# Kernel optimization log

Hardware: AMD Instinct MI355X
Metric: run time of the kernel (lower is better)

Reference implementation:

```python
import jax, jax.numpy as jnp
import numpy as np

L, D, H, KVH, DH, F, V, SMAX, T = 4, 2048, 16, 8, 128, 6144, 32000, 2048, 1024
EPS = 1e-6
ROPE_THETA = 1e6


def rotate_half(x, axis=-1):
    x1, x2 = jnp.split(x, 2, axis=axis)
    return jnp.concatenate((-x2, x1), axis=axis)


def rms(x, w):
    return w * (x / jnp.sqrt(jnp.mean(x * x, axis=-1, keepdims=True) + EPS))


def setup_inputs() -> dict:
    key = jax.random.key(0)
    ks = jax.random.split(key, 16)
    s = 0.02
    inv_freq = 1.0 / (ROPE_THETA ** (jnp.arange(0, DH, 2, dtype=jnp.float32) / DH))
    ang = jnp.arange(SMAX, dtype=jnp.float32)[:, None] * inv_freq[None, :]  # [SMAX, DH/2]
    cos_emb = jnp.concatenate([jnp.cos(ang), jnp.cos(ang)], axis=-1)  # [SMAX, DH]
    sin_emb = jnp.concatenate([jnp.sin(ang), jnp.sin(ang)], axis=-1)
    sf = DH ** (-0.25)  # scale_factor pre-baked into q_norm/k_norm weights
    return {
        "key_buffer": jnp.zeros((L, KVH, 1, DH, SMAX), jnp.float32),
        "value_buffer": jnp.zeros((L, KVH, 1, SMAX, DH), jnp.float32),
        "input_ids": jax.random.randint(ks[0], (1, T), 0, V, dtype=jnp.int32),
        "attention_mask": jnp.ones((1, T, T), jnp.float32),
        "past_len": 0,
        "embed_data": jax.random.randint(ks[1], (V, D), 0, 256).astype(jnp.uint8),
        "embed_scale": jax.random.uniform(ks[2], (V, 1), jnp.float32, 0.001, 0.02),
        "embed_zero": jax.random.normal(ks[3], (V, 1), jnp.float32) * 0.1,
        "cos_emb": cos_emb,
        "sin_emb": sin_emb,
        "w_in_ln": jnp.ones((L, D), jnp.float32),
        "Wq": jax.random.normal(ks[4], (L, D, H * DH), jnp.float32) * s,
        "Wk": jax.random.normal(ks[5], (L, D, KVH * DH), jnp.float32) * s,
        "Wv": jax.random.normal(ks[6], (L, D, KVH * DH), jnp.float32) * s,
        "w_q_norm": jnp.full((L, DH), sf, jnp.float32),
        "w_k_norm": jnp.full((L, DH), sf, jnp.float32),
        "Wo": jax.random.normal(ks[7], (L, H * DH, D), jnp.float32) * s,
        "w_post_ln": jnp.ones((L, D), jnp.float32),
        "Wgate": jax.random.normal(ks[8], (L, D, F), jnp.float32) * s,
        "Wup": jax.random.normal(ks[9], (L, D, F), jnp.float32) * s,
        "Wdown": jax.random.normal(ks[10], (L, F, D), jnp.float32) * s,
        "w_final_norm": jnp.ones((D,), jnp.float32),
        "W_lm": jax.random.normal(ks[11], (D, V), jnp.float32) * s,
    }


def reference(key_buffer, value_buffer, input_ids, attention_mask, past_len,
              embed_data, embed_scale, embed_zero, cos_emb, sin_emb,
              w_in_ln, Wq, Wk, Wv, w_q_norm, w_k_norm, Wo, w_post_ln,
              Wgate, Wup, Wdown, w_final_norm, W_lm):
    new_len = input_ids.shape[1]
    end = past_len + new_len  # static (past_len is a Python int)
    cos_q = cos_emb[past_len:end]  # [T, DH]
    sin_q = sin_emb[past_len:end]
    # uint8 embedding dequant: e * scale + zero_point
    hidden = embed_data[input_ids].astype(jnp.float32) * embed_scale[input_ids] + embed_zero[input_ids]  # [1,T,D]
    # causal mask: (1 - tril) * -128, sliced to [1, new_len, end], times user mask
    rows = jnp.arange(new_len) + past_len
    cols = jnp.arange(end)
    mask = jnp.where(cols[None, :] <= rows[:, None], 0.0, -128.0)[None] * attention_mask  # [1,T,end]
    G = H // KVH
    for i in range(L):
        hn = rms(hidden, w_in_ln[i])[0]  # [T, D]
        q = (hn @ Wq[i]).reshape(new_len, H, DH)
        q = jnp.transpose(rms(q, w_q_norm[i]), (1, 0, 2))  # [H,T,DH] (sqrt(scale) baked in w_q_norm)
        k = (hn @ Wk[i]).reshape(new_len, KVH, DH)
        k = jnp.transpose(rms(k, w_k_norm[i]), (1, 2, 0))  # [KVH,DH,T]
        v = jnp.transpose((hn @ Wv[i]).reshape(new_len, KVH, DH), (1, 0, 2))  # [KVH,T,DH]
        # RoPE on keys (rotate along DH axis=1)
        k = k * cos_q.T + rotate_half(k, axis=1) * sin_q.T
        key_buffer = jax.lax.dynamic_update_slice(key_buffer, k[None, :, None], (i, 0, 0, 0, past_len))
        value_buffer = jax.lax.dynamic_update_slice(value_buffer, v[None, :, None], (i, 0, 0, past_len, 0))
        # GQA expand: each kv head repeated G times consecutively
        k_exp = jnp.repeat(key_buffer[i, :, 0, :, :end], G, axis=0)  # [H,DH,end]
        v_exp = jnp.repeat(value_buffer[i, :, 0, :end, :], G, axis=0)  # [H,end,DH]
        q_rot = q * cos_q[None] + rotate_half(q, axis=-1) * sin_q[None]
        scores = jnp.einsum('htd,hds->hts', q_rot, k_exp) + mask
        attn = jax.nn.softmax(scores, axis=-1)
        ctx = jnp.transpose(jnp.einsum('hts,hsd->htd', attn, v_exp), (1, 0, 2)).reshape(1, new_len, H * DH)
        hidden = hidden + ctx @ Wo[i]
        hn2 = rms(hidden, w_post_ln[i])
        hidden = hidden + (jax.nn.silu(hn2 @ Wgate[i]) * (hn2 @ Wup[i])) @ Wdown[i]
    last = rms(hidden[:, -1], w_final_norm)  # [1, D]
    logits = last @ W_lm  # [1, V]
    tok_id = jnp.argmax(logits, axis=-1, keepdims=True).astype(jnp.int32)
    new_seq_len = jnp.array([end], dtype=jnp.int32)
    return (tok_id, key_buffer, value_buffer, new_seq_len)
```

## Files before the change

kernel.cpp:

```cpp
#include <hip/hip_runtime.h>
#include <cstdint>

#define L_ 4
#define D_ 2048
#define H_ 16
#define KVH_ 8
#define DH_ 128
#define F_ 6144
#define V_ 32000
#define SMAX_ 2048
#define T_ 1024
#define EPS_ 1e-6f
#define QB 32
#define SB 128
#define ZSE 4194304

typedef unsigned short u16;
typedef unsigned int u32;
typedef float fvec4 __attribute__((ext_vector_type(4)));
typedef float f32x4 __attribute__((ext_vector_type(4)));
typedef __bf16 bf16x8 __attribute__((ext_vector_type(8)));

__device__ __forceinline__ u16 f2bf(float f) {
  union { float f; u32 u; } a; a.f = f;
  u32 u = a.u;
  return (u16)((u + 0x7FFFu + ((u >> 16) & 1u)) >> 16);
}

__device__ __forceinline__ void gld16(const void* g, void* l) {
  __builtin_amdgcn_global_load_lds(
      (const __attribute__((address_space(1))) void*)g,
      (__attribute__((address_space(3))) void*)l, 16, 0, 0);
}

__device__ __forceinline__ float blk_sum(float v, volatile float* sm) {
#pragma unroll
  for (int m = 32; m; m >>= 1) v += __shfl_xor(v, m);
  if ((threadIdx.x & 63) == 0) sm[threadIdx.x >> 6] = v;
  __syncthreads();
  v = sm[0] + sm[1] + sm[2] + sm[3];
  __syncthreads();
  return v;
}

__global__ void embed_k(const int* __restrict__ ids, const void* __restrict__ edata,
                        const float* __restrict__ esc, const float* __restrict__ ez,
                        float* __restrict__ hidden)
{
  const int* ei = (const int*)edata;
  int chk = ei[threadIdx.x & 63];
  bool ok = ((unsigned)chk) <= 255u;
  bool is_i32 = (__ballot(ok) == ~0ULL);
  int t = blockIdx.x;
  int id = ids[t];
  float sc = esc[id], zp = ez[id];
  size_t base = (size_t)id * D_;
  const uint8_t* eb = (const uint8_t*)edata;
  for (int d = threadIdx.x; d < D_; d += 256) {
    float e = is_i32 ? (float)ei[base + d] : (float)eb[base + d];
    hidden[(size_t)t * D_ + d] = e * sc + zp;
  }
}

__global__ __launch_bounds__(256)
void convT2_k(const float* __restrict__ W0, const float* __restrict__ W1,
              const float* __restrict__ W2,
              int x1, int x2, int N0, int N1, int N2,
              int r0, int r1, int r2, int K, u16* __restrict__ WT, int gu)
{
  __shared__ float tile[64][65];
  int x = blockIdx.x, k0 = blockIdx.y * 64;
  const float* W; int N, nb, rb;
  if (x < x1)      { W = W0; N = N0; nb = x;      rb = r0; }
  else if (x < x2) { W = W1; N = N1; nb = x - x1; rb = r1; }
  else             { W = W2; N = N2; nb = x - x2; rb = r2; }
  int n0 = nb * 64;
  int tid = threadIdx.x;
  int lk = tid >> 4, n4 = (tid & 15) * 4;
#pragma unroll
  for (int i = 0; i < 4; ++i) {
    int kr = i * 16 + lk;
    fvec4 v = *(const fvec4*)(W + (size_t)(k0 + kr) * N + n0 + n4);
#pragma unroll
    for (int j = 0; j < 4; ++j) tile[n4 + j][kr] = v[j];
  }
  __syncthreads();
  int n = tid >> 2, kq = (tid & 3) * 16;
  int f = n0 + n;
  int row = gu ? (rb + ((f >> 4) << 5) + (f & 15)) : (rb + f);
  union { u16 h[16]; uint4 q[2]; } o;
#pragma unroll
  for (int i = 0; i < 16; ++i) o.h[i] = f2bf(tile[n][kq + i]);
  u16* op = WT + (size_t)row * K + k0 + kq;
  *(uint4*)op = o.q[0];
  *(uint4*)(op + 8) = o.q[1];
}

template<int NZ>
__global__ __launch_bounds__(256)
void rms_k(float* __restrict__ x, const float* __restrict__ p,
           const float* __restrict__ w, u16* __restrict__ out)
{
  int t = blockIdx.x * 4 + (threadIdx.x >> 6);
  int l = threadIdx.x & 63;
  fvec4* xr = (fvec4*)(x + (size_t)t * D_);
  fvec4 v[8];
#pragma unroll
  for (int j = 0; j < 8; ++j) v[j] = xr[l + 64 * j];
  if (NZ > 0) {
#pragma unroll
    for (int z = 0; z < NZ; ++z) {
      const fvec4* a = (const fvec4*)(p + (size_t)z * ZSE + (size_t)t * D_);
#pragma unroll
      for (int j = 0; j < 8; ++j) v[j] += a[l + 64 * j];
    }
#pragma unroll
    for (int j = 0; j < 8; ++j) xr[l + 64 * j] = v[j];
  }
  float s = 0.f;
#pragma unroll
  for (int j = 0; j < 8; ++j)
    s += v[j][0]*v[j][0] + v[j][1]*v[j][1] + v[j][2]*v[j][2] + v[j][3]*v[j][3];
#pragma unroll
  for (int m = 32; m; m >>= 1) s += __shfl_xor(s, m);
  float inv = rsqrtf(s * (1.f / D_) + EPS_);
  const fvec4* wr = (const fvec4*)w;
  u16* orow = out + (size_t)t * D_;
#pragma unroll
  for (int j = 0; j < 8; ++j) {
    fvec4 wv = wr[l + 64 * j];
    uint2 o;
    o.x = (u32)f2bf(wv[0]*v[j][0]*inv) | ((u32)f2bf(wv[1]*v[j][1]*inv) << 16);
    o.y = (u32)f2bf(wv[2]*v[j][2]*inv) | ((u32)f2bf(wv[3]*v[j][3]*inv) << 16);
    *(uint2*)(orow + (l + 64 * j) * 4) = o;
  }
}

template<int EPI>
__global__ __launch_bounds__(256)
void gemm_bt(const u16* __restrict__ A, const u16* __restrict__ B,
             float* __restrict__ Cf, u16* __restrict__ Cb,
             int K, int Ks, int ldC, long long zStride)
{
  __shared__ u16 lA[128 * 64];
  __shared__ u16 lB[128 * 64];
  const u16* Ab = A + (size_t)blockIdx.y * 128 * K;
  const u16* Bb = B + (size_t)blockIdx.x * 128 * K;
  int kz = blockIdx.z * Ks;

  int tid = threadIdx.x;
  int l = tid & 63;
  int wid = tid >> 6;
  int wr = wid >> 1, wc = wid & 1;
  int lrow = l & 15, lk = l >> 4;

  f32x4 acc[4][4] = {};

  for (int k0 = 0; k0 < Ks; k0 += 64) {
#pragma unroll
    for (int r = 0; r < 4; ++r) {
      int c = r * 256 + tid;
      int row = c >> 3, g = c & 7;
      int kel = kz + k0 + ((g ^ (row & 7)) << 3);
      gld16(Ab + (size_t)row * K + kel, (char*)lA + c * 16);
      gld16(Bb + (size_t)row * K + kel, (char*)lB + c * 16);
    }
    __syncthreads();
#pragma unroll
    for (int kk = 0; kk < 2; ++kk) {
      bf16x8 av[4], bv[4];
      int kbyte = (kk * 32 + lk * 8) * 2;
#pragma unroll
      for (int m = 0; m < 4; ++m) {
        int row = wr * 64 + m * 16 + lrow;
        int byt = (row * 128 + kbyte) ^ ((row & 7) << 4);
        av[m] = *(const bf16x8*)((const char*)lA + byt);
      }
#pragma unroll
      for (int n = 0; n < 4; ++n) {
        int row = wc * 64 + n * 16 + lrow;
        int byt = (row * 128 + kbyte) ^ ((row & 7) << 4);
        bv[n] = *(const bf16x8*)((const char*)lB + byt);
      }
#pragma unroll
      for (int m = 0; m < 4; ++m)
#pragma unroll
        for (int n = 0; n < 4; ++n)
          acc[m][n] = __builtin_amdgcn_mfma_f32_16x16x32_bf16(av[m], bv[n], acc[m][n], 0, 0, 0);
    }
    __syncthreads();
  }

  int grow0 = blockIdx.y * 128 + wr * 64 + lk * 4;
  if (EPI == 3) {
    int fcol0 = blockIdx.x * 64 + wc * 32 + lrow;
#pragma unroll
    for (int m = 0; m < 4; ++m)
#pragma unroll
      for (int np = 0; np < 2; ++np)
#pragma unroll
        for (int r = 0; r < 4; ++r) {
          float g = acc[m][2 * np][r], u = acc[m][2 * np + 1][r];
          float val = g / (1.f + __expf(-g)) * u;
          Cb[(size_t)(grow0 + m * 16 + r) * ldC + fcol0 + np * 16] = f2bf(val);
        }
    return;
  }
  float* Cz = Cf + (long long)blockIdx.z * zStride;
  int gcol0 = blockIdx.x * 128 + wc * 64 + lrow;
#pragma unroll
  for (int m = 0; m < 4; ++m)
#pragma unroll
    for (int n = 0; n < 4; ++n)
#pragma unroll
      for (int r = 0; r < 4; ++r) {
        size_t off = (size_t)(grow0 + m * 16 + r) * ldC + gcol0 + n * 16;
        Cz[off] = acc[m][n][r];
      }
}

__global__ __launch_bounds__(256)
void qkvpost_k(const float* __restrict__ p0, const float* __restrict__ p1,
               const float* __restrict__ wq, const float* __restrict__ wk,
               const float* __restrict__ cosT, const float* __restrict__ sinT,
               const int* __restrict__ plp,
               u16* __restrict__ qr, u16* __restrict__ kr, u16* __restrict__ vT,
               float* __restrict__ key_out, float* __restrict__ val_out)
{
  __shared__ float tile[64][132];
  int t0 = blockIdx.x * 64;
  int z = blockIdx.y;
  int pl = plp[0];
  int tid = threadIdx.x;
  int cb = z < 16 ? z * 128 : (z < 24 ? 2048 + (z - 16) * 128 : 3072 + (z - 24) * 128);

  {
    int r = tid >> 5;
    int c = (tid & 31) * 4;
#pragma unroll
    for (int i = 0; i < 8; ++i) {
      int row = i * 8 + r;
      size_t off = (size_t)(t0 + row) * 4096 + cb + c;
      fvec4 v = *(const fvec4*)(p0 + off) + *(const fvec4*)(p1 + off);
      *(fvec4*)&tile[row][c] = v;
    }
  }
  __syncthreads();

  if (z < 24) {
    int row = tid >> 2, q = tid & 3;
    int dbase = q * 32, pbase = (q ^ 2) * 32;
    const float* wn = z < 16 ? wq : wk;
    float sgn = (q < 2) ? -1.f : 1.f;
    fvec4 xv[8];
    float ss = 0.f;
#pragma unroll
    for (int j = 0; j < 8; ++j) {
      xv[j] = *(const fvec4*)&tile[row][dbase + j * 4];
      ss += xv[j][0]*xv[j][0] + xv[j][1]*xv[j][1] + xv[j][2]*xv[j][2] + xv[j][3]*xv[j][3];
    }
    ss += __shfl_xor(ss, 1);
    ss += __shfl_xor(ss, 2);
    float inv = rsqrtf(ss * (1.f / 128.f) + EPS_);
    int p = pl + t0 + row;
    float rv[32];
#pragma unroll
    for (int j = 0; j < 8; ++j) {
      fvec4 xo = *(const fvec4*)&tile[row][pbase + j * 4];
      fvec4 wv = *(const fvec4*)(wn + dbase + j * 4);
      fvec4 wo = *(const fvec4*)(wn + pbase + j * 4);
      fvec4 cs = *(const fvec4*)(cosT + (size_t)p * 128 + dbase + j * 4);
      fvec4 sn = *(const fvec4*)(sinT + (size_t)p * 128 + dbase + j * 4);
#pragma unroll
      for (int e = 0; e < 4; ++e) {
        float xn = wv[e] * xv[j][e] * inv;
        float xp = wo[e] * xo[e] * inv;
        rv[j * 4 + e] = xn * cs[e] + sgn * xp * sn[e];
      }
    }
    union { u32 w[8]; uint4 q4[2]; } ob;
    u16* orow = (z < 16 ? qr + ((size_t)z * T_ + t0 + row) * 128
                        : kr + ((size_t)(z - 16) * T_ + t0 + row) * 128) + dbase;
#pragma unroll
    for (int j = 0; j < 8; ++j)
      ob.w[j] = (u32)f2bf(rv[2 * j]) | ((u32)f2bf(rv[2 * j + 1]) << 16);
    *(uint4*)orow = ob.q4[0];
    *(uint4*)(orow + 8) = ob.q4[1];
#pragma unroll
    for (int j = 0; j < 8; ++j)
      ob.w[j] = (u32)f2bf(rv[16 + 2 * j]) | ((u32)f2bf(rv[17 + 2 * j]) << 16);
    *(uint4*)(orow + 16) = ob.q4[0];
    *(uint4*)(orow + 24) = ob.q4[1];

    if (z >= 16) {
      __syncthreads();
#pragma unroll
      for (int j = 0; j < 8; ++j) {
        fvec4 v; v[0] = rv[j*4]; v[1] = rv[j*4+1]; v[2] = rv[j*4+2]; v[3] = rv[j*4+3];
        *(fvec4*)&tile[row][dbase + j * 4] = v;
      }
      __syncthreads();
      int d = tid >> 1, cc = (tid & 1) * 32;
      float* kp = key_out + ((size_t)(z - 16) * 128 + d) * SMAX_ + pl + t0 + cc;
      if ((pl & 3) == 0) {
#pragma unroll
        for (int j4 = 0; j4 < 8; ++j4) {
          fvec4 v;
#pragma unroll
          for (int e = 0; e < 4; ++e) v[e] = tile[cc + j4 * 4 + e][d];
          *(fvec4*)(kp + j4 * 4) = v;
        }
      } else {
        for (int j = 0; j < 32; ++j) kp[j] = tile[cc + j][d];
      }
    }
  } else {
    int kv = z - 24;
    int row = tid >> 2, q = tid & 3;
    float* vp = val_out + ((size_t)kv * SMAX_ + pl + t0 + row) * 128 + q * 32;
#pragma unroll
    for (int j = 0; j < 8; ++j)
      *(fvec4*)(vp + j * 4) = *(const fvec4*)&tile[row][q * 32 + j * 4];
    int d = tid >> 1, cc = (tid & 1) * 32;
    union { u32 w[16]; uint4 q4[4]; } ob;
    u16* tp = vT + ((size_t)kv * 128 + d) * T_ + t0 + cc;
#pragma unroll
    for (int j = 0; j < 16; ++j)
      ob.w[j] = (u32)f2bf(tile[cc + 2 * j][d]) | ((u32)f2bf(tile[cc + 2 * j + 1][d]) << 16);
    *(uint4*)tp = ob.q4[0];
    *(uint4*)(tp + 8) = ob.q4[1];
    *(uint4*)(tp + 16) = ob.q4[2];
    *(uint4*)(tp + 24) = ob.q4[3];
  }
}

__global__ __launch_bounds__(256)
void flash_k(const u16* __restrict__ qr, const u16* __restrict__ kr,
             const u16* __restrict__ vTb, const float* __restrict__ am,
             const int* __restrict__ plp, u16* __restrict__ ctx)
{
  __shared__ u16 lQ[QB * DH_];
  __shared__ u16 lKV[SB * DH_];
  __shared__ u16 lP[QB * SB];
  __shared__ float lMax[2][2][16];
  __shared__ float lSum[2][2][16];
  __shared__ float lScale[QB];
  __shared__ float lFin[QB];

  int qt = gridDim.x - 1 - blockIdx.x;
  int h = blockIdx.y;
  int kvh = h >> 1;
  int pl = plp[0];
  int tid = threadIdx.x;
  int l = tid & 63, w = tid >> 6;
  int lrow = l & 15, lk = l >> 4;
  int tb = w & 1, sh = w >> 1;
  int tcol = tb * 16 + lrow;

  const u16* Qb = qr + ((size_t)h * T_ + qt * QB) * DH_;
  const u16* Kb = kr + (size_t)kvh * T_ * DH_;
  const u16* Vb = vTb + (size_t)kvh * DH_ * T_;

#pragma unroll
  for (int r = 0; r < 2; ++r) {
    int c = r * 256 + tid;
    int row = c >> 4, g = c & 15;
    gld16(Qb + (size_t)row * DH_ + ((g ^ (row & 7)) << 3), (char*)lQ + c * 16);
  }

  float m_run = -3.0e38f, l_run = 0.f;
  f32x4 acc_o[2][2] = {};

  int t_lo = qt * QB;
  int s_hi = min(T_, t_lo + QB + pl);
  int nt = (s_hi + SB - 1) / SB;
  int tg = t_lo + tcol;

  for (int it = 0; it < nt; ++it) {
    int s0 = it * SB;
#pragma unroll
    for (int r = 0; r < 8; ++r) {
      int c = r * 256 + tid;
      int row = c >> 4, g = c & 15;
      gld16(Kb + (size_t)(s0 + row) * DH_ + ((g ^ (row & 7)) << 3), (char*)lKV + c * 16);
    }
    __syncthreads();

    f32x4 acc_s[4] = {};
#pragma unroll
    for (int kk = 0; kk < 4; ++kk) {
      int kbyte = kk * 64 + lk * 16;
      int trow = tb * 16 + lrow;
      bf16x8 bq = *(const bf16x8*)((const char*)lQ + ((trow * 256 + kbyte) ^ ((trow & 7) << 4)));
#pragma unroll
      for (int m = 0; m < 4; ++m) {
        int srow = sh * 64 + m * 16 + lrow;
        bf16x8 ak = *(const bf16x8*)((const char*)lKV + ((srow * 256 + kbyte) ^ ((srow & 7) << 4)));
        acc_s[m] = __builtin_amdgcn_mfma_f32_16x16x32_bf16(ak, bq, acc_s[m], 0, 0, 0);
      }
    }
    __syncthreads();

#pragma unroll
    for (int r = 0; r < 8; ++r) {
      int c = r * 256 + tid;
      int row = c >> 4, g = c & 15;
      gld16(Vb + (size_t)row * T_ + s0 + ((g ^ (row & 7)) << 3), (char*)lKV + c * 16);
    }

    bool full = (s0 + SB <= t_lo + pl + 1);
    float sv[4][4];
    float vmax = -3.0e38f;
    if (full) {
#pragma unroll
      for (int m = 0; m < 4; ++m)
#pragma unroll
        for (int r = 0; r < 4; ++r) {
          float val = acc_s[m][r]; sv[m][r] = val; vmax = fmaxf(vmax, val);
        }
    } else {
#pragma unroll
      for (int m = 0; m < 4; ++m) {
        int sg = s0 + sh * 64 + m * 16 + lk * 4;
        fvec4 a4 = *(const fvec4*)(am + (size_t)tg * T_ + sg);
#pragma unroll
        for (int r = 0; r < 4; ++r) {
          float val = acc_s[m][r] + ((sg + r <= tg + pl) ? 0.f : -128.f * a4[r]);
          sv[m][r] = val; vmax = fmaxf(vmax, val);
        }
      }
    }
    vmax = fmaxf(vmax, __shfl_xor(vmax, 16));
    vmax = fmaxf(vmax, __shfl_xor(vmax, 32));
    if (lk == 0) lMax[tb][sh][lrow] = vmax;
    __syncthreads();

    float om = fmaxf(lMax[tb][0][lrow], lMax[tb][1][lrow]);
    float m_new = fmaxf(m_run, om);
    float corr = __expf(m_run - m_new);
    float psum = 0.f;
    u32 pw[4][2];
#pragma unroll
    for (int m = 0; m < 4; ++m) {
      float p0 = __expf(sv[m][0] - m_new);
      float p1 = __expf(sv[m][1] - m_new);
      float p2 = __expf(sv[m][2] - m_new);
      float p3 = __expf(sv[m][3] - m_new);
      psum += (p0 + p1) + (p2 + p3);
      pw[m][0] = (u32)f2bf(p0) | ((u32)f2bf(p1) << 16);
      pw[m][1] = (u32)f2bf(p2) | ((u32)f2bf(p3) << 16);
    }
    psum += __shfl_xor(psum, 16);
    psum += __shfl_xor(psum, 32);
    if (lk == 0) lSum[tb][sh][lrow] = psum;
    if (lk == 0 && sh == 0) lScale[tcol] = corr;
#pragma unroll
    for (int m = 0; m < 4; ++m) {
      int byt = (tcol * 256 + sh * 128 + m * 32 + lk * 8) ^ ((tcol & 7) << 4);
      *(uint2*)((char*)lP + byt) = make_uint2(pw[m][0], pw[m][1]);
    }
    __syncthreads();

    l_run = l_run * corr + lSum[tb][0][lrow] + lSum[tb][1][lrow];
    m_run = m_new;
#pragma unroll
    for (int m = 0; m < 2; ++m) {
      fvec4 c4 = *(const fvec4*)&lScale[m * 16 + lk * 4];
#pragma unroll
      for (int n = 0; n < 2; ++n)
#pragma unroll
        for (int r = 0; r < 4; ++r) acc_o[m][n][r] *= c4[r];
    }
#pragma unroll
    for (int kk = 0; kk < 4; ++kk) {
      int kbyte = kk * 64 + lk * 16;
      bf16x8 ap[2], bv[2];
#pragma unroll
      for (int m = 0; m < 2; ++m) {
        int trow = m * 16 + lrow;
        ap[m] = *(const bf16x8*)((const char*)lP + ((trow * 256 + kbyte) ^ ((trow & 7) << 4)));
      }
#pragma unroll
      for (int n = 0; n < 2; ++n) {
        int drow = w * 32 + n * 16 + lrow;
        bv[n] = *(const bf16x8*)((const char*)lKV + ((drow * 256 + kbyte) ^ ((drow & 7) << 4)));
      }
#pragma unroll
      for (int m = 0; m < 2; ++m)
#pragma unroll
        for (int n = 0; n < 2; ++n)
          acc_o[m][n] = __builtin_amdgcn_mfma_f32_16x16x32_bf16(ap[m], bv[n], acc_o[m][n], 0, 0, 0);
    }
    __syncthreads();
  }

  if (lk == 0 && sh == 0) lFin[tcol] = l_run;
  __syncthreads();
#pragma unroll
  for (int m = 0; m < 2; ++m) {
    fvec4 s4 = *(const fvec4*)&lFin[m * 16 + lk * 4];
#pragma unroll
    for (int r = 0; r < 4; ++r) {
      float inv = 1.f / s4[r];
      int trow = t_lo + m * 16 + lk * 4 + r;
      u16* crow = ctx + (size_t)trow * (H_ * DH_) + h * DH_;
#pragma unroll
      for (int n = 0; n < 2; ++n) {
        int d = w * 32 + n * 16 + lrow;
        crow[d] = f2bf(acc_o[m][n][r] * inv);
      }
    }
  }
}

__global__ void frms_k(const float* __restrict__ x, const float* __restrict__ p,
                       const float* __restrict__ w, float* __restrict__ out)
{
  __shared__ float sm[4];
  float s = 0.f;
  for (int d = threadIdx.x; d < D_; d += 256) {
    float v = x[d] + p[d] + p[ZSE + d] + p[2 * ZSE + d] + p[3 * ZSE + d];
    s += v * v;
  }
  s = blk_sum(s, sm);
  float inv = rsqrtf(s * (1.f / D_) + EPS_);
  for (int d = threadIdx.x; d < D_; d += 256)
    out[d] = w[d] * (x[d] + p[d] + p[ZSE + d] + p[2 * ZSE + d] + p[3 * ZSE + d]) * inv;
}

__global__ void lmgemv_k(const float* __restrict__ last, const float* __restrict__ Wlm,
                         float* __restrict__ part)
{
  __shared__ float ls[256];
  int v = blockIdx.x * 256 + threadIdx.x;
  int c = blockIdx.y;
  ls[threadIdx.x] = last[c * 256 + threadIdx.x];
  __syncthreads();
  const float* Wp = Wlm + (size_t)c * 256 * V_ + v;
  float acc = 0.f;
#pragma unroll 8
  for (int d = 0; d < 256; d++) acc += ls[d] * Wp[(size_t)d * V_];
  part[(size_t)c * V_ + v] = acc;
}

__global__ void amax_part_k(const float* __restrict__ part, float2* __restrict__ out)
{
  __shared__ float sv[4];
  __shared__ int si[4];
  int v = blockIdx.x * 256 + threadIdx.x;
  float val = 0.f;
#pragma unroll
  for (int c = 0; c < 8; c++) val += part[(size_t)c * V_ + v];
  float bv = val; int bi = v;
#pragma unroll
  for (int m = 32; m; m >>= 1) {
    float ov = __shfl_xor(bv, m);
    int oi = __shfl_xor(bi, m);
    if (ov > bv || (ov == bv && oi < bi)) { bv = ov; bi = oi; }
  }
  if ((threadIdx.x & 63) == 0) { sv[threadIdx.x >> 6] = bv; si[threadIdx.x >> 6] = bi; }
  __syncthreads();
  if (threadIdx.x == 0) {
    for (int w = 1; w < 4; w++)
      if (sv[w] > bv || (sv[w] == bv && si[w] < bi)) { bv = sv[w]; bi = si[w]; }
    out[blockIdx.x] = make_float2(bv, (float)bi);
  }
}

__global__ void finalize_k(const float2* __restrict__ part, int np,
                           const int* __restrict__ plp, float* __restrict__ dout,
                           unsigned long long lastoff)
{
  if (threadIdx.x == 0) {
    float bv = part[0].x; int bi = (int)part[0].y;
    for (int b = 1; b < np; b++) {
      float v = part[b].x; int i = (int)part[b].y;
      if (v > bv || (v == bv && i < bi)) { bv = v; bi = i; }
    }
    dout[0] = (float)bi;
    dout[lastoff] = (float)(plp[0] + T_);
  }
}

extern "C" void kernel_launch(void* const* d_in, const int* in_sizes, int n_in,
                              void* d_out, int out_size, void* d_ws, size_t ws_size,
                              hipStream_t stream)
{
  (void)in_sizes; (void)n_in; (void)out_size; (void)ws_size;

  const float* key_in  = (const float*)d_in[0];
  const float* val_in  = (const float*)d_in[1];
  const int*   ids     = (const int*)d_in[2];
  const float* am      = (const float*)d_in[3];
  const int*   plp     = (const int*)d_in[4];
  const void*  edata   = d_in[5];
  const float* esc     = (const float*)d_in[6];
  const float* ez      = (const float*)d_in[7];
  const float* cosT    = (const float*)d_in[8];
  const float* sinT    = (const float*)d_in[9];
  const float* w_in_ln = (const float*)d_in[10];
  const float* Wq      = (const float*)d_in[11];
  const float* Wk      = (const float*)d_in[12];
  const float* Wv      = (const float*)d_in[13];
  const float* wqn     = (const float*)d_in[14];
  const float* wkn     = (const float*)d_in[15];
  const float* Wo      = (const float*)d_in[16];
  const float* wpost   = (const float*)d_in[17];
  const float* Wg      = (const float*)d_in[18];
  const float* Wu      = (const float*)d_in[19];
  const float* Wd      = (const float*)d_in[20];
  const float* wfin    = (const float*)d_in[21];
  const float* Wlm     = (const float*)d_in[22];

  float* out = (float*)d_out;
  const size_t KVN = (size_t)L_ * KVH_ * DH_ * SMAX_;
  float* key_out = out + 1;
  float* val_out = out + 1 + KVN;
  unsigned long long lastoff = 1 + 2 * KVN;

  char* ws = (char*)d_ws;
  u16*   wT     = (u16*)  (ws + 0);
  u16*   hn     = (u16*)  (ws + 50331648);
  float* P      = (float*)(ws + 54525952);
  u16*   qr     = (u16*)  (ws + 121634816);
  u16*   kr     = (u16*)  (ws + 125829120);
  u16*   vT     = (u16*)  (ws + 127926272);
  u16*   ctx    = (u16*)  (ws + 130023424);
  float* hidden = (float*)(ws + 134217728);
  u16*   mlp    = (u16*)  (ws + 142606336);
  float* last   = (float*)(ws + 155189248);
  float* lpart  = (float*)(ws + 155197440);
  float2* amaxp = (float2*)(ws + 156221440);

  hipMemcpyAsync(key_out, key_in, KVN * sizeof(float), hipMemcpyDeviceToDevice, stream);
  hipMemcpyAsync(val_out, val_in, KVN * sizeof(float), hipMemcpyDeviceToDevice, stream);
  embed_k<<<T_, 256, 0, stream>>>(ids, edata, esc, ez, hidden);

  for (int i = 0; i < L_; i++) {
    if (i == 0)
      rms_k<0><<<T_ / 4, 256, 0, stream>>>(hidden, nullptr, w_in_ln, hn);
    else
      rms_k<4><<<T_ / 4, 256, 0, stream>>>(hidden, P, w_in_ln + (size_t)i * D_, hn);

    convT2_k<<<dim3(64, 32), 256, 0, stream>>>(
        Wq + (size_t)i * 4194304, Wk + (size_t)i * 2097152, Wv + (size_t)i * 2097152,
        32, 48, 2048, 1024, 1024, 0, 2048, 3072, 2048, wT, 0);
    gemm_bt<0><<<dim3(32, 8, 2), 256, 0, stream>>>(hn, wT, P, nullptr, 2048, 1024, 4096, ZSE);

    qkvpost_k<<<dim3(T_ / 64, 32), 256, 0, stream>>>(P, P + ZSE,
        wqn + (size_t)i * DH_, wkn + (size_t)i * DH_, cosT, sinT, plp,
        qr, kr, vT,
        key_out + (size_t)i * KVH_ * DH_ * SMAX_,
        val_out + (size_t)i * KVH_ * SMAX_ * DH_);

    flash_k<<<dim3(T_ / QB, H_), 256, 0, stream>>>(qr, kr, vT, am, plp, ctx);

    convT2_k<<<dim3(32, 32), 256, 0, stream>>>(
        Wo + (size_t)i * 4194304, nullptr, nullptr,
        32, 64, 2048, 2048, 2048, 0, 0, 0, 2048, wT, 0);
    gemm_bt<0><<<dim3(16, 8, 4), 256, 0, stream>>>(ctx, wT, P, nullptr, 2048, 512, 2048, ZSE);

    rms_k<4><<<T_ / 4, 256, 0, stream>>>(hidden, P, wpost + (size_t)i * D_, hn);

    convT2_k<<<dim3(192, 32), 256, 0, stream>>>(
        Wg + (size_t)i * 12582912, Wu + (size_t)i * 12582912, Wu + (size_t)i * 12582912,
        96, 192, 6144, 6144, 6144, 0, 16, 16, 2048, wT, 1);
    gemm_bt<3><<<dim3(96, 8, 1), 256, 0, stream>>>(hn, wT, nullptr, mlp, 2048, 2048, 6144, 0);

    convT2_k<<<dim3(32, 96), 256, 0, stream>>>(
        Wd + (size_t)i * 12582912, nullptr, nullptr,
        32, 64, 2048, 2048, 2048, 0, 0, 0, 6144, wT, 0);
    gemm_bt<0><<<dim3(16, 8, 4), 256, 0, stream>>>(mlp, wT, P, nullptr, 6144, 1536, 2048, ZSE);
  }

  frms_k<<<1, 256, 0, stream>>>(hidden + (size_t)(T_ - 1) * D_,
                                P + (size_t)(T_ - 1) * D_, wfin, last);
  lmgemv_k<<<dim3(V_ / 256, 8), 256, 0, stream>>>(last, Wlm, lpart);
  amax_part_k<<<V_ / 256, 256, 0, stream>>>(lpart, amaxp);
  finalize_k<<<1, 64, 0, stream>>>(amaxp, V_ / 256, plp, out, lastoff);
}
```

Before: 1.201 ms.

## Fuse weight transposes with RMS/qkv-post kernels and store split-K partials in bf16

```diff
diff --git a/kernel.cpp b/kernel.cpp
--- a/kernel.cpp
+++ b/kernel.cpp
@@ -26,21 +26,20 @@
   u32 u = a.u;
   return (u16)((u + 0x7FFFu + ((u >> 16) & 1u)) >> 16);
 }
+__device__ __forceinline__ float bf2f(u16 h) {
+  union { u32 u; float f; } a; a.u = (u32)h << 16; return a.f;
+}
+__device__ __forceinline__ fvec4 bf4(uint2 u) {
+  union { u32 i; float f; } a, b, c, d;
+  a.i = u.x << 16; b.i = u.x & 0xFFFF0000u;
+  c.i = u.y << 16; d.i = u.y & 0xFFFF0000u;
+  fvec4 r; r[0] = a.f; r[1] = b.f; r[2] = c.f; r[3] = d.f; return r;
+}
 
 __device__ __forceinline__ void gld16(const void* g, void* l) {
   __builtin_amdgcn_global_load_lds(
       (const __attribute__((address_space(1))) void*)g,
       (__attribute__((address_space(3))) void*)l, 16, 0, 0);
-}
-
-__device__ __forceinline__ float blk_sum(float v, volatile float* sm) {
-#pragma unroll
-  for (int m = 32; m; m >>= 1) v += __shfl_xor(v, m);
-  if ((threadIdx.x & 63) == 0) sm[threadIdx.x >> 6] = v;
-  __syncthreads();
-  v = sm[0] + sm[1] + sm[2] + sm[3];
-  __syncthreads();
-  return v;
 }
 
 __global__ void embed_k(const int* __restrict__ ids, const void* __restrict__ edata,
@@ -62,19 +61,11 @@
   }
 }
 
-__global__ __launch_bounds__(256)
-void convT2_k(const float* __restrict__ W0, const float* __restrict__ W1,
-              const float* __restrict__ W2,
-              int x1, int x2, int N0, int N1, int N2,
-              int r0, int r1, int r2, int K, u16* __restrict__ WT, int gu)
-{
-  __shared__ float tile[64][65];
-  int x = blockIdx.x, k0 = blockIdx.y * 64;
-  const float* W; int N, nb, rb;
-  if (x < x1)      { W = W0; N = N0; nb = x;      rb = r0; }
-  else if (x < x2) { W = W1; N = N1; nb = x - x1; rb = r1; }
-  else             { W = W2; N = N2; nb = x - x2; rb = r2; }
-  int n0 = nb * 64;
+__device__ __forceinline__ void convT_body(const float* __restrict__ W, int N,
+                                           int nb, int kb, int K, int rb,
+                                           u16* __restrict__ WT, int gu, float* tile)
+{
+  int n0 = nb * 64, k0 = kb * 64;
   int tid = threadIdx.x;
   int lk = tid >> 4, n4 = (tid & 15) * 4;
 #pragma unroll
@@ -82,7 +73,7 @@
     int kr = i * 16 + lk;
     fvec4 v = *(const fvec4*)(W + (size_t)(k0 + kr) * N + n0 + n4);
 #pragma unroll
-    for (int j = 0; j < 4; ++j) tile[n4 + j][kr] = v[j];
+    for (int j = 0; j < 4; ++j) tile[(n4 + j) * 65 + kr] = v[j];
   }
   __syncthreads();
   int n = tid >> 2, kq = (tid & 3) * 16;
@@ -90,18 +81,19 @@
   int row = gu ? (rb + ((f >> 4) << 5) + (f & 15)) : (rb + f);
   union { u16 h[16]; uint4 q[2]; } o;
 #pragma unroll
-  for (int i = 0; i < 16; ++i) o.h[i] = f2bf(tile[n][kq + i]);
+  for (int i = 0; i < 16; ++i) o.h[i] = f2bf(tile[n * 65 + kq + i]);
   u16* op = WT + (size_t)row * K + k0 + kq;
   *(uint4*)op = o.q[0];
   *(uint4*)(op + 8) = o.q[1];
 }
 
 template<int NZ>
-__global__ __launch_bounds__(256)
-void rms_k(float* __restrict__ x, const float* __restrict__ p,
-           const float* __restrict__ w, u16* __restrict__ out)
-{
-  int t = blockIdx.x * 4 + (threadIdx.x >> 6);
+__device__ __forceinline__ void rms_body(int idx, float* __restrict__ x,
+                                         const u16* __restrict__ p,
+                                         const float* __restrict__ w,
+                                         u16* __restrict__ out)
+{
+  int t = idx * 4 + (threadIdx.x >> 6);
   int l = threadIdx.x & 63;
   fvec4* xr = (fvec4*)(x + (size_t)t * D_);
   fvec4 v[8];
@@ -110,9 +102,9 @@
   if (NZ > 0) {
 #pragma unroll
     for (int z = 0; z < NZ; ++z) {
-      const fvec4* a = (const fvec4*)(p + (size_t)z * ZSE + (size_t)t * D_);
-#pragma unroll
-      for (int j = 0; j < 8; ++j) v[j] += a[l + 64 * j];
+      const uint2* a = (const uint2*)(p + (size_t)z * ZSE + (size_t)t * D_);
+#pragma unroll
+      for (int j = 0; j < 8; ++j) v[j] += bf4(a[l + 64 * j]);
     }
 #pragma unroll
     for (int j = 0; j < 8; ++j) xr[l + 64 * j] = v[j];
@@ -136,11 +128,52 @@
   }
 }
 
+template<int NZ>
+__global__ __launch_bounds__(256)
+void convqkv_rms_k(const float* __restrict__ Wq, const float* __restrict__ Wk,
+                   const float* __restrict__ Wv, u16* __restrict__ WT,
+                   float* __restrict__ x, const u16* __restrict__ p,
+                   const float* __restrict__ w, u16* __restrict__ out)
+{
+  __shared__ float tile[64 * 65];
+  int bx = blockIdx.x, y = blockIdx.y;
+  if (bx < 64) {
+    const float* W; int N, nb, rb;
+    if (bx < 32)      { W = Wq; N = 2048; nb = bx;      rb = 0; }
+    else if (bx < 48) { W = Wk; N = 1024; nb = bx - 32; rb = 2048; }
+    else              { W = Wv; N = 1024; nb = bx - 48; rb = 3072; }
+    convT_body(W, N, nb, y, 2048, rb, WT, 0, tile);
+  } else {
+    rms_body<NZ>((bx - 64) * 32 + y, x, p, w, out);
+  }
+}
+
+__global__ __launch_bounds__(256)
+void convgu_wd_rms_k(const float* __restrict__ Wg, const float* __restrict__ Wu,
+                     u16* __restrict__ WTgu, const float* __restrict__ Wd,
+                     u16* __restrict__ WTwd,
+                     float* __restrict__ x, const u16* __restrict__ p,
+                     const float* __restrict__ w, u16* __restrict__ out)
+{
+  __shared__ float tile[64 * 65];
+  int bx = blockIdx.x, y = blockIdx.y;
+  if (bx < 192) {
+    const float* W; int nb, rb;
+    if (bx < 96) { W = Wg; nb = bx;      rb = 0; }
+    else         { W = Wu; nb = bx - 96; rb = 16; }
+    convT_body(W, 6144, nb, y, 2048, rb, WTgu, 1, tile);
+  } else if (bx < 288) {
+    int xp = bx - 192;
+    convT_body(Wd, 2048, xp & 31, ((xp >> 5) << 5) + y, 6144, 0, WTwd, 0, tile);
+  } else {
+    rms_body<4>((bx - 288) * 32 + y, x, p, w, out);
+  }
+}
+
 template<int EPI>
 __global__ __launch_bounds__(256)
 void gemm_bt(const u16* __restrict__ A, const u16* __restrict__ B,
-             float* __restrict__ Cf, u16* __restrict__ Cb,
-             int K, int Ks, int ldC, long long zStride)
+             u16* __restrict__ Cb, int K, int Ks, int ldC, long long zStride)
 {
   __shared__ u16 lA[128 * 64];
   __shared__ u16 lB[128 * 64];
@@ -206,28 +239,31 @@
         }
     return;
   }
-  float* Cz = Cf + (long long)blockIdx.z * zStride;
+  u16* Cz = Cb + (long long)blockIdx.z * zStride;
   int gcol0 = blockIdx.x * 128 + wc * 64 + lrow;
 #pragma unroll
   for (int m = 0; m < 4; ++m)
 #pragma unroll
     for (int n = 0; n < 4; ++n)
 #pragma unroll
-      for (int r = 0; r < 4; ++r) {
-        size_t off = (size_t)(grow0 + m * 16 + r) * ldC + gcol0 + n * 16;
-        Cz[off] = acc[m][n][r];
-      }
+      for (int r = 0; r < 4; ++r)
+        Cz[(size_t)(grow0 + m * 16 + r) * ldC + gcol0 + n * 16] = f2bf(acc[m][n][r]);
 }
 
 __global__ __launch_bounds__(256)
-void qkvpost_k(const float* __restrict__ p0, const float* __restrict__ p1,
-               const float* __restrict__ wq, const float* __restrict__ wk,
-               const float* __restrict__ cosT, const float* __restrict__ sinT,
-               const int* __restrict__ plp,
-               u16* __restrict__ qr, u16* __restrict__ kr, u16* __restrict__ vT,
-               float* __restrict__ key_out, float* __restrict__ val_out)
+void qkvpost_convwo_k(const u16* __restrict__ p0, const u16* __restrict__ p1,
+                      const float* __restrict__ wq, const float* __restrict__ wk,
+                      const float* __restrict__ cosT, const float* __restrict__ sinT,
+                      const int* __restrict__ plp,
+                      u16* __restrict__ qr, u16* __restrict__ kr, u16* __restrict__ vT,
+                      float* __restrict__ key_out, float* __restrict__ val_out,
+                      const float* __restrict__ Wo, u16* __restrict__ WTo)
 {
   __shared__ float tile[64][132];
+  if (blockIdx.x >= 16) {
+    convT_body(Wo, 2048, blockIdx.x - 16, blockIdx.y, 2048, 0, WTo, 0, &tile[0][0]);
+    return;
+  }
   int t0 = blockIdx.x * 64;
   int z = blockIdx.y;
   int pl = plp[0];
@@ -241,7 +277,7 @@
     for (int i = 0; i < 8; ++i) {
       int row = i * 8 + r;
       size_t off = (size_t)(t0 + row) * 4096 + cb + c;
-      fvec4 v = *(const fvec4*)(p0 + off) + *(const fvec4*)(p1 + off);
+      fvec4 v = bf4(*(const uint2*)(p0 + off)) + bf4(*(const uint2*)(p1 + off));
       *(fvec4*)&tile[row][c] = v;
     }
   }
@@ -513,19 +549,23 @@
   }
 }
 
-__global__ void frms_k(const float* __restrict__ x, const float* __restrict__ p,
+__global__ void frms_k(const float* __restrict__ x, const u16* __restrict__ p,
                        const float* __restrict__ w, float* __restrict__ out)
 {
   __shared__ float sm[4];
   float s = 0.f;
   for (int d = threadIdx.x; d < D_; d += 256) {
-    float v = x[d] + p[d] + p[ZSE + d] + p[2 * ZSE + d] + p[3 * ZSE + d];
+    float v = x[d] + bf2f(p[d]) + bf2f(p[ZSE + d]) + bf2f(p[2 * ZSE + d]) + bf2f(p[3 * ZSE + d]);
     s += v * v;
   }
-  s = blk_sum(s, sm);
+#pragma unroll
+  for (int m = 32; m; m >>= 1) s += __shfl_xor(s, m);
+  if ((threadIdx.x & 63) == 0) sm[threadIdx.x >> 6] = s;
+  __syncthreads();
+  s = sm[0] + sm[1] + sm[2] + sm[3];
   float inv = rsqrtf(s * (1.f / D_) + EPS_);
   for (int d = threadIdx.x; d < D_; d += 256)
-    out[d] = w[d] * (x[d] + p[d] + p[ZSE + d] + p[2 * ZSE + d] + p[3 * ZSE + d]) * inv;
+    out[d] = w[d] * (x[d] + bf2f(p[d]) + bf2f(p[ZSE + d]) + bf2f(p[2 * ZSE + d]) + bf2f(p[3 * ZSE + d])) * inv;
 }
 
 __global__ void lmgemv_k(const float* __restrict__ last, const float* __restrict__ Wlm,
@@ -620,17 +660,18 @@
 
   char* ws = (char*)d_ws;
   u16*   wT     = (u16*)  (ws + 0);
-  u16*   hn     = (u16*)  (ws + 50331648);
-  float* P      = (float*)(ws + 54525952);
-  u16*   qr     = (u16*)  (ws + 121634816);
-  u16*   kr     = (u16*)  (ws + 125829120);
-  u16*   vT     = (u16*)  (ws + 127926272);
-  u16*   ctx    = (u16*)  (ws + 130023424);
-  float* hidden = (float*)(ws + 134217728);
-  u16*   mlp    = (u16*)  (ws + 142606336);
-  float* last   = (float*)(ws + 155189248);
-  float* lpart  = (float*)(ws + 155197440);
-  float2* amaxp = (float2*)(ws + 156221440);
+  u16*   wTwd   = wT + 25165824;
+  u16*   hn     = (u16*)  (ws + 75497472);
+  u16*   P      = (u16*)  (ws + 79691776);
+  u16*   qr     = (u16*)  (ws + 113246208);
+  u16*   kr     = (u16*)  (ws + 117440512);
+  u16*   vT     = (u16*)  (ws + 119537664);
+  u16*   ctx    = (u16*)  (ws + 121634816);
+  float* hidden = (float*)(ws + 125829120);
+  u16*   mlp    = (u16*)  (ws + 134217728);
+  float* last   = (float*)(ws + 146800640);
+  float* lpart  = (float*)(ws + 146808832);
+  float2* amaxp = (float2*)(ws + 147832832);
 
   hipMemcpyAsync(key_out, key_in, KVN * sizeof(float), hipMemcpyDeviceToDevice, stream);
   hipMemcpyAsync(val_out, val_in, KVN * sizeof(float), hipMemcpyDeviceToDevice, stream);
@@ -638,39 +679,34 @@
 
   for (int i = 0; i < L_; i++) {
     if (i == 0)
-      rms_k<0><<<T_ / 4, 256, 0, stream>>>(hidden, nullptr, w_in_ln, hn);
+      convqkv_rms_k<0><<<dim3(72, 32), 256, 0, stream>>>(
+          Wq, Wk, Wv, wT, hidden, nullptr, w_in_ln, hn);
     else
-      rms_k<4><<<T_ / 4, 256, 0, stream>>>(hidden, P, w_in_ln + (size_t)i * D_, hn);
-
-    convT2_k<<<dim3(64, 32), 256, 0, stream>>>(
-        Wq + (size_t)i * 4194304, Wk + (size_t)i * 2097152, Wv + (size_t)i * 2097152,
-        32, 48, 2048, 1024, 1024, 0, 2048, 3072, 2048, wT, 0);
-    gemm_bt<0><<<dim3(32, 8, 2), 256, 0, stream>>>(hn, wT, P, nullptr, 2048, 1024, 4096, ZSE);
-
-    qkvpost_k<<<dim3(T_ / 64, 32), 256, 0, stream>>>(P, P + ZSE,
+      convqkv_rms_k<4><<<dim3(72, 32), 256, 0, stream>>>(
+          Wq + (size_t)i * 4194304, Wk + (size_t)i * 2097152, Wv + (size_t)i * 2097152,
+          wT, hidden, P, w_in_ln + (size_t)i * D_, hn);
+
+    gemm_bt<0><<<dim3(32, 8, 2), 256, 0, stream>>>(hn, wT, P, 2048, 1024, 4096, ZSE);
+
+    qkvpost_convwo_k<<<dim3(48, 32), 256, 0, stream>>>(P, P + ZSE,
         wqn + (size_t)i * DH_, wkn + (size_t)i * DH_, cosT, sinT, plp,
         qr, kr, vT,
         key_out + (size_t)i * KVH_ * DH_ * SMAX_,
-        val_out + (size_t)i * KVH_ * SMAX_ * DH_);
+        val_out + (size_t)i * KVH_ * SMAX_ * DH_,
+        Wo + (size_t)i * 4194304, wT);
 
     flash_k<<<dim3(T_ / QB, H_), 256, 0, stream>>>(qr, kr, vT, am, plp, ctx);
 
-    convT2_k<<<dim3(32, 32), 256, 0, stream>>>(
-        Wo + (size_t)i * 4194304, nullptr, nullptr,
-        32, 64, 2048, 2048, 2048, 0, 0, 0, 2048, wT, 0);
-    gemm_bt<0><<<dim3(16, 8, 4), 256, 0, stream>>>(ctx, wT, P, nullptr, 2048, 512, 2048, ZSE);
-
-    rms_k<4><<<T_ / 4, 256, 0, stream>>>(hidden, P, wpost + (size_t)i * D_, hn);
-
-    convT2_k<<<dim3(192, 32), 256, 0, stream>>>(
-        Wg + (size_t)i * 12582912, Wu + (size_t)i * 12582912, Wu + (size_t)i * 12582912,
-        96, 192, 6144, 6144, 6144, 0, 16, 16, 2048, wT, 1);
-    gemm_bt<3><<<dim3(96, 8, 1), 256, 0, stream>>>(hn, wT, nullptr, mlp, 2048, 2048, 6144, 0);
-
-    convT2_k<<<dim3(32, 96), 256, 0, stream>>>(
-        Wd + (size_t)i * 12582912, nullptr, nullptr,
-        32, 64, 2048, 2048, 2048, 0, 0, 0, 6144, wT, 0);
-    gemm_bt<0><<<dim3(16, 8, 4), 256, 0, stream>>>(mlp, wT, P, nullptr, 6144, 1536, 2048, ZSE);
+    gemm_bt<0><<<dim3(16, 8, 4), 256, 0, stream>>>(ctx, wT, P, 2048, 512, 2048, ZSE);
+
+    convgu_wd_rms_k<<<dim3(296, 32), 256, 0, stream>>>(
+        Wg + (size_t)i * 12582912, Wu + (size_t)i * 12582912, wT,
+        Wd + (size_t)i * 12582912, wTwd,
+        hidden, P, wpost + (size_t)i * D_, hn);
+
+    gemm_bt<3><<<dim3(96, 8, 1), 256, 0, stream>>>(hn, wT, mlp, 2048, 2048, 6144, 0);
+
+    gemm_bt<0><<<dim3(16, 8, 4), 256, 0, stream>>>(mlp, wTwd, P, 6144, 1536, 2048, ZSE);
   }
 
   frms_k<<<1, 256, 0, stream>>>(hidden + (size_t)(T_ - 1) * D_,
```

After: 1.133 ms. -5.6%, faster.
